# Performance work log

Hardware: AMD Instinct MI355X
Metric: run time of the kernel (lower is better)

The kernel has to match this reference:

```python
import jax, jax.numpy as jnp
import numpy as np

B, K = 4, 128
V_IN, V_OUT = 256, 256
E_IN, E_OUT = 512, 512
P_PE, T_PE = 200, 100
HEADS = 16  # c_atten_head


def _lin(key, din, dout):
    kw, kb = jax.random.split(key)
    W = jax.random.normal(kw, (din, dout), jnp.float32) / np.sqrt(din).astype(np.float32)
    b = jax.random.normal(kb, (dout,), jnp.float32) * 0.01
    return W, b


def setup_inputs() -> dict:
    key = jax.random.key(0)
    ks = jax.random.split(key, 14)
    v_f = jax.random.normal(ks[0], (B, K, V_IN), jnp.float32)
    e_f = jax.random.normal(ks[1], (B, K * K, E_IN), jnp.float32)
    p_pe = jax.random.normal(ks[2], (B, K, P_PE), jnp.float32)
    t_pe = jax.random.normal(ks[3], (B, T_PE), jnp.float32)
    e_agg_mask = (jax.random.uniform(ks[4], (B, K, K)) > 0.1).astype(jnp.float32)
    v_agg_mask = (jax.random.uniform(ks[5], (B, K)) > 0.1).astype(jnp.float32)
    W_vpe, b_vpe = _lin(ks[6], V_IN + P_PE + T_PE, V_IN)
    W_epe, b_epe = _lin(ks[7], E_IN + T_PE, E_IN)
    W_ev1, b_ev1 = _lin(ks[8], E_IN + 2 * V_IN, E_OUT)
    W_ev2, b_ev2 = _lin(ks[9], E_OUT, E_OUT)
    W_q, b_q = _lin(ks[10], V_IN, E_OUT)
    W_k, b_k = _lin(ks[11], V_IN, E_OUT)
    W_self, b_self = _lin(ks[12], V_IN, E_OUT)
    W_out, b_out = _lin(ks[13], 2 * E_OUT, V_OUT)
    return dict(v_f=v_f, e_f=e_f, p_pe=p_pe, t_pe=t_pe,
                e_agg_mask=e_agg_mask, v_agg_mask=v_agg_mask,
                W_vpe=W_vpe, b_vpe=b_vpe, W_epe=W_epe, b_epe=b_epe,
                W_ev1=W_ev1, b_ev1=b_ev1, W_ev2=W_ev2, b_ev2=b_ev2,
                W_q=W_q, b_q=b_q, W_k=W_k, b_k=b_k,
                W_self=W_self, b_self=b_self, W_out=W_out, b_out=b_out)


def reference(v_f, e_f, p_pe, t_pe, e_agg_mask, v_agg_mask,
              W_vpe, b_vpe, W_epe, b_epe, W_ev1, b_ev1, W_ev2, b_ev2,
              W_q, b_q, W_k, b_k, W_self, b_self, W_out, b_out):
    silu = jax.nn.silu
    # PE binding
    t_v = jnp.broadcast_to(t_pe[:, None, :], (B, K, T_PE))
    v = silu(jnp.concatenate([v_f, p_pe, t_v], -1) @ W_vpe + b_vpe)          # (B,K,V_IN)
    t_e = jnp.broadcast_to(t_pe[:, None, :], (B, K * K, T_PE))
    e = silu(jnp.concatenate([e_f, t_e], -1) @ W_epe + b_epe)                # (B,K*K,E_IN)
    # dense all-pairs node features -> edge values
    pair = jnp.concatenate([jnp.broadcast_to(v[:, :, None, :], (B, K, K, V_IN)),
                            jnp.broadcast_to(v[:, None, :, :], (B, K, K, V_IN))], -1)
    ev_in = jnp.concatenate([pair.reshape(B, K * K, 2 * V_IN), e], -1)
    e_value = silu(ev_in @ W_ev1 + b_ev1) @ W_ev2 + b_ev2                     # (B,K*K,E_OUT)
    agg_e = e_value.reshape(B, K, K, E_OUT)
    # elementwise-multiply / head-sum attention
    q = v @ W_q + b_q                                                         # (B,K,E_OUT)
    k = v @ W_k + b_k
    att = (q[:, :, None, :] * k[:, None, :, :]).reshape(B, K, K, E_OUT // HEADS, HEADS)
    att = att.sum(-1, keepdims=True) / np.float32(np.sqrt(HEADS * 3.0))       # (B,K,K,G,1)
    a = jax.nn.sigmoid(att) * e_agg_mask[..., None, None]
    a = a / (a.sum(2, keepdims=True) + 1e-6)
    a = jnp.broadcast_to(a, (B, K, K, E_OUT // HEADS, HEADS)).reshape(B, K, K, E_OUT)
    agg_v = (a * agg_e).sum(2)                                                # (B,K,E_OUT)
    v2 = agg_v + silu(v @ W_self + b_self)
    # masked max-pool over nodes
    pooled = (v2 - 1e9 * (1.0 - v_agg_mask)[..., None]).max(1, keepdims=True)
    pooled = jnp.broadcast_to(pooled, (B, K, E_OUT))
    v_out = silu(jnp.concatenate([v2, pooled], -1) @ W_out + b_out)           # (B,K,V_OUT)
    return v_out, e_value
```

## Files before the change

kernel.cpp:

```cpp
#include <hip/hip_runtime.h>

typedef unsigned short ushort_t;
typedef __attribute__((ext_vector_type(8))) short bf16x8;
typedef __attribute__((ext_vector_type(4))) float f32x4;

__device__ __forceinline__ ushort_t f2bf(float f) {
    union { float f; unsigned u; } v; v.f = f;
    unsigned r = v.u + 0x7FFFu + ((v.u >> 16) & 1u);
    return (ushort_t)(r >> 16);
}
__device__ __forceinline__ float siluf(float x) { return x / (1.f + __expf(-x)); }
__device__ __forceinline__ float sigm(float x)  { return 1.f / (1.f + __expf(-x)); }

__device__ __forceinline__ void gl2lds16(const void* g, void* l) {
    __builtin_amdgcn_global_load_lds(
        (__attribute__((address_space(1))) void*)(const_cast<void*>(g)),
        (__attribute__((address_space(3))) void*)(l), 16, 0, 0);
}


__global__ void k_prep(const float* t_pe, const float* W_vpe, const float* b_vpe,
                       const float* W_epe, const float* b_epe,
                       float* c_v, float* c_e) {
    int b = blockIdx.x, t = threadIdx.x;
    {
        float acc = b_epe[t];
        for (int u = 0; u < 100; ++u) acc += t_pe[b*100+u] * W_epe[(512+u)*512 + t];
        c_e[b*512 + t] = acc;
    }
    if (t < 256) {
        float acc = b_vpe[t];
        for (int u = 0; u < 100; ++u) acc += t_pe[b*100+u] * W_vpe[(456+u)*256 + t];
        c_v[b*256 + t] = acc;
    }
}

__global__ void k_transpose(const float* W_epe, const float* W_ev1, const float* W_ev2,
                            ushort_t* WT_epe, ushort_t* WT_c, ushort_t* WT_ev2) {
    int n = blockIdx.x;
    int mat = blockIdx.y;
    const float* src; ushort_t* dst;
    if (mat == 0)      { src = W_epe;            dst = WT_epe; }
    else if (mat == 1) { src = W_ev1 + 512*512;  dst = WT_c;   }
    else               { src = W_ev2;            dst = WT_ev2; }
    for (int k = threadIdx.x; k < 512; k += 256)
        dst[n*512 + k] = f2bf(src[k*512 + n]);
}

__global__ __launch_bounds__(256) void k_cvt(const float* src, ushort_t* dst) {
    size_t id = (size_t)blockIdx.x * 256 + threadIdx.x;
    const float4* s = (const float4*)src + id * 2;
    float4 a = s[0], b = s[1];
    ushort4* d = (ushort4*)dst + id * 2;
    d[0] = make_ushort4(f2bf(a.x), f2bf(a.y), f2bf(a.z), f2bf(a.w));
    d[1] = make_ushort4(f2bf(b.x), f2bf(b.y), f2bf(b.z), f2bf(b.w));
}

__global__ void k_node_v(const float* v_f, const float* p_pe, const float* W_vpe,
                         const float* c_v, float* v) {
    __shared__ float rv[4][256];
    __shared__ float rp[4][200];
    int r0 = blockIdx.x * 4, t = threadIdx.x;
    for (int rr = 0; rr < 4; ++rr) {
        rv[rr][t] = v_f[(r0+rr)*256 + t];
        if (t < 200) rp[rr][t] = p_pe[(r0+rr)*200 + t];
    }
    __syncthreads();
    int b = r0 >> 7;
    float acc[4];
    float cv = c_v[b*256 + t];
    for (int rr = 0; rr < 4; ++rr) acc[rr] = cv;
    for (int k = 0; k < 256; ++k) {
        float w = W_vpe[k*256 + t];
        #pragma unroll
        for (int rr = 0; rr < 4; ++rr) acc[rr] += rv[rr][k] * w;
    }
    for (int k = 0; k < 200; ++k) {
        float w = W_vpe[(256+k)*256 + t];
        #pragma unroll
        for (int rr = 0; rr < 4; ++rr) acc[rr] += rp[rr][k] * w;
    }
    for (int rr = 0; rr < 4; ++rr) v[(r0+rr)*256 + t] = siluf(acc[rr]);
}

__global__ void k_node_proj(const float* v,
                            const float* W_q, const float* b_q,
                            const float* W_k, const float* b_k,
                            const float* W_self, const float* b_self,
                            const float* W_ev1, const float* b_ev1,
                            float* q, float* kk, float* vs, float* P, float* Q) {
    __shared__ float rv[4][256];
    int r0 = blockIdx.x * 4, which = blockIdx.y, t = threadIdx.x;
    for (int rr = 0; rr < 4; ++rr) rv[rr][t] = v[(r0+rr)*256 + t];
    __syncthreads();
    const float* W; const float* bias = nullptr; float* out; bool do_silu = false;
    if (which == 0)      { W = W_q;    bias = b_q;    out = q;  }
    else if (which == 1) { W = W_k;    bias = b_k;    out = kk; }
    else if (which == 2) { W = W_self; bias = b_self; out = vs; do_silu = true; }
    else if (which == 3) { W = W_ev1;  bias = b_ev1;  out = P;  }
    else                 { W = W_ev1 + 256*512;       out = Q;  }
    float acc[4][2] = {};
    for (int k = 0; k < 256; ++k) {
        float w0 = W[k*512 + t];
        float w1 = W[k*512 + t + 256];
        #pragma unroll
        for (int rr = 0; rr < 4; ++rr) {
            acc[rr][0] += rv[rr][k] * w0;
            acc[rr][1] += rv[rr][k] * w1;
        }
    }
    float bb0 = bias ? bias[t] : 0.f;
    float bb1 = bias ? bias[t + 256] : 0.f;
    for (int rr = 0; rr < 4; ++rr) {
        float x0 = acc[rr][0] + bb0;
        float x1 = acc[rr][1] + bb1;
        if (do_silu) { x0 = siluf(x0); x1 = siluf(x1); }
        out[(r0+rr)*512 + t]       = x0;
        out[(r0+rr)*512 + t + 256] = x1;
    }
}

__global__ __launch_bounds__(256) void k_attw(const float* q, const float* kmat,
                                              const float* emask, float* anorm) {
    int bi = blockIdx.x; int b = bi >> 7, i = bi & 127;
    int t = threadIdx.x;
    __shared__ __align__(16) float qrow[512];
    __shared__ float s[128][33];
    __shared__ float invd[32];
    qrow[t]       = q[(size_t)bi*512 + t];
    qrow[t + 256] = q[(size_t)bi*512 + t + 256];
    __syncthreads();
    {
        int j = t >> 1, g0 = (t & 1) * 16;
        const float* kr = kmat + ((size_t)b*128 + j) * 512;
        float msk = emask[(size_t)b*16384 + i*128 + j];
        for (int gg = 0; gg < 16; ++gg) {
            int g = g0 + gg;
            const float4* k4 = (const float4*)(kr + g*16);
            const float4* q4 = (const float4*)(qrow + g*16);
            float acc = 0.f;
            #pragma unroll
            for (int c = 0; c < 4; ++c) {
                float4 kv = k4[c], qv = q4[c];
                acc += kv.x*qv.x + kv.y*qv.y + kv.z*qv.z + kv.w*qv.w;
            }
            s[j][g] = sigm(acc * 0.14433756729740645f) * msk;
        }
    }
    __syncthreads();
    if (t < 32) {
        float d = 1e-6f;
        for (int j = 0; j < 128; ++j) d += s[j][t];
        invd[t] = 1.f / d;
    }
    __syncthreads();
    float* dst = anorm + (size_t)bi * 4096;
    for (int idx = t; idx < 4096; idx += 256) {
        int j = idx >> 5, g = idx & 31;
        dst[idx] = s[j][g] * invd[g];
    }
}

template <int MODE>
__global__ __launch_bounds__(256) void k_gemm(const ushort_t* A, const ushort_t* BT,
                                              const float* e0, const float* e1,
                                              const float* e2,
                                              ushort_t* out16, float* out32,
                                              float* v2out) {
    __shared__ __align__(16) ushort_t As[128*32];
    __shared__ __align__(16) ushort_t Bs[128*32];
    __shared__ float aw[(MODE == 2) ? 4096 : 4];
    __shared__ float red[(MODE == 2) ? 256 : 4];

    int lin = blockIdx.x;
    int xcd = lin & 7, idx = lin >> 3;
    int mt = xcd * 64 + (idx >> 2);
    int nt = idx & 3;
    int m0 = mt * 128, n0 = nt * 128;
    int t = threadIdx.x;
    int wv = t >> 6, lane = t & 63;
    int wm = (wv >> 1) * 64, wn = (wv & 1) * 64;
    int ml = lane & 15, quad = lane >> 4;
    f32x4 acc[4][4] = {};

    if (MODE == 2) {
        const float4* src = (const float4*)(e1 + (size_t)mt * 4096);
        float4* dst = (float4*)aw;
        for (int i = t; i < 1024; i += 256) dst[i] = src[i];
    }

    int srow = t >> 2, sseg = t & 3;
    const ushort_t* gA0 = A + (size_t)(m0 + srow) * 512 + sseg * 8;
    const ushort_t* gA1 = A + (size_t)(m0 + 64 + srow) * 512 + sseg * 8;
    const ushort_t* gB0 = BT + (size_t)(n0 + srow) * 512 + sseg * 8;
    const ushort_t* gB1 = BT + (size_t)(n0 + 64 + srow) * 512 + sseg * 8;
    ushort_t* lA0 = As + wv * 512;
    ushort_t* lA1 = As + 2048 + wv * 512;
    ushort_t* lB0 = Bs + wv * 512;
    ushort_t* lB1 = Bs + 2048 + wv * 512;

    for (int kk = 0; kk < 512; kk += 32) {
        gl2lds16(gA0 + kk, lA0);
        gl2lds16(gA1 + kk, lA1);
        gl2lds16(gB0 + kk, lB0);
        gl2lds16(gB1 + kk, lB1);
        __syncthreads();
        bf16x8 a[4], b[4];
        #pragma unroll
        for (int tm = 0; tm < 4; ++tm)
            a[tm] = *(const bf16x8*)(As + (wm + tm*16 + ml) * 32 + quad * 8);
        #pragma unroll
        for (int tn = 0; tn < 4; ++tn)
            b[tn] = *(const bf16x8*)(Bs + (wn + tn*16 + ml) * 32 + quad * 8);
        #pragma unroll
        for (int tm = 0; tm < 4; ++tm)
            #pragma unroll
            for (int tn = 0; tn < 4; ++tn)
                acc[tm][tn] = __builtin_amdgcn_mfma_f32_16x16x32_bf16(a[tm], b[tn], acc[tm][tn], 0, 0, 0);
        __syncthreads();
    }

    if (MODE == 2) {
        float partial[4] = {0.f, 0.f, 0.f, 0.f};
        #pragma unroll
        for (int tm = 0; tm < 4; ++tm)
            #pragma unroll
            for (int tn = 0; tn < 4; ++tn)
                #pragma unroll
                for (int r = 0; r < 4; ++r) {
                    int j  = wm + tm*16 + quad*4 + r;
                    int gn = n0 + wn + tn*16 + ml;
                    float x = acc[tm][tn][r] + e0[gn];
                    out32[((size_t)m0 + j) * 512 + gn] = x;
                    partial[tn] += aw[j * 32 + (gn >> 4)] * x;
                }
        #pragma unroll
        for (int tn = 0; tn < 4; ++tn) {
            float p = partial[tn];
            p += __shfl_down(p, 32);
            p += __shfl_down(p, 16);
            if (quad == 0 && lane < 16) red[wv * 64 + tn * 16 + ml] = p;
        }
        __syncthreads();
        if (t < 128) {
            int c = t, half = c >> 6, cl = c & 63;
            float tot = red[half * 64 + cl] + red[(half + 2) * 64 + cl];
            size_t o = (size_t)mt * 512 + n0 + c;
            v2out[o] = tot + e2[o];
        }
    } else {
        #pragma unroll
        for (int tm = 0; tm < 4; ++tm)
            #pragma unroll
            for (int tn = 0; tn < 4; ++tn)
                #pragma unroll
                for (int r = 0; r < 4; ++r) {
                    int gm = m0 + wm + tm*16 + quad*4 + r;
                    int gn = n0 + wn + tn*16 + ml;
                    float x = acc[tm][tn][r];
                    if (MODE == 0) {
                        x += e0[(gm >> 14) * 512 + gn];
                    } else {
                        int b_ = gm >> 14, ij = gm & 16383, i = ij >> 7, j = ij & 127;
                        x += e0[(size_t)((b_ << 7) + i) * 512 + gn]
                           + e1[(size_t)((b_ << 7) + j) * 512 + gn];
                    }
                    out16[(size_t)gm * 512 + gn] = f2bf(siluf(x));
                }
    }
}

__global__ void k_pool(const float* v2, const float* vmask, const float* W_out,
                       const float* b_out, float* cpool) {
    int b = blockIdx.x, t = threadIdx.x;
    __shared__ float pooled[512];
    for (int d = t; d < 512; d += 256) {
        float m = -1e30f;
        for (int i = 0; i < 128; ++i) {
            float val = v2[((size_t)(b*128 + i))*512 + d] - 1e9f * (1.f - vmask[b*128 + i]);
            m = fmaxf(m, val);
        }
        pooled[d] = m;
    }
    __syncthreads();
    float acc = b_out[t];
    for (int d = 0; d < 512; ++d) acc += pooled[d] * W_out[(512 + d)*256 + t];
    cpool[b*256 + t] = acc;
}

__global__ void k_node_out(const float* v2, const float* W_out, const float* cpool,
                           float* out) {
    __shared__ float rv[4][512];
    int r0 = blockIdx.x * 4, t = threadIdx.x;
    for (int rr = 0; rr < 4; ++rr) {
        rv[rr][t]       = v2[(size_t)(r0+rr)*512 + t];
        rv[rr][t + 256] = v2[(size_t)(r0+rr)*512 + t + 256];
    }
    __syncthreads();
    int b = r0 >> 7;
    float acc[4];
    float cp = cpool[b*256 + t];
    for (int rr = 0; rr < 4; ++rr) acc[rr] = cp;
    for (int k = 0; k < 512; ++k) {
        float w = W_out[k*256 + t];
        #pragma unroll
        for (int rr = 0; rr < 4; ++rr) acc[rr] += rv[rr][k] * w;
    }
    for (int rr = 0; rr < 4; ++rr) out[(r0+rr)*256 + t] = siluf(acc[rr]);
}

extern "C" void kernel_launch(void* const* d_in, const int* in_sizes, int n_in,
                              void* d_out, int out_size, void* d_ws, size_t ws_size,
                              hipStream_t stream) {
    const float* v_f    = (const float*)d_in[0];
    const float* e_f    = (const float*)d_in[1];
    const float* p_pe   = (const float*)d_in[2];
    const float* t_pe   = (const float*)d_in[3];
    const float* emask  = (const float*)d_in[4];
    const float* vmask  = (const float*)d_in[5];
    const float* W_vpe  = (const float*)d_in[6];
    const float* b_vpe  = (const float*)d_in[7];
    const float* W_epe  = (const float*)d_in[8];
    const float* b_epe  = (const float*)d_in[9];
    const float* W_ev1  = (const float*)d_in[10];
    const float* b_ev1  = (const float*)d_in[11];
    const float* W_ev2  = (const float*)d_in[12];
    const float* b_ev2  = (const float*)d_in[13];
    const float* W_q    = (const float*)d_in[14];
    const float* b_q    = (const float*)d_in[15];
    const float* W_k    = (const float*)d_in[16];
    const float* b_k    = (const float*)d_in[17];
    const float* W_self = (const float*)d_in[18];
    const float* b_self = (const float*)d_in[19];
    const float* W_out  = (const float*)d_in[20];
    const float* b_out  = (const float*)d_in[21];

    float* out_v = (float*)d_out;
    float* out_e = (float*)d_out + 131072;

    char* w = (char*)d_ws;
    ushort_t* WT_epe = (ushort_t*)w; w += 512*512*2;
    ushort_t* WT_c   = (ushort_t*)w; w += 512*512*2;
    ushort_t* WT_ev2 = (ushort_t*)w; w += 512*512*2;
    float* c_v   = (float*)w; w += 4*256*4;
    float* c_e   = (float*)w; w += 4*512*4;
    float* v     = (float*)w; w += 512*256*4;
    float* qbuf  = (float*)w; w += 512*512*4;
    float* kbuf  = (float*)w; w += 512*512*4;
    float* vsbuf = (float*)w; w += 512*512*4;
    float* Pbuf  = (float*)w; w += 512*512*4;
    float* Qbuf  = (float*)w; w += 512*512*4;
    float* v2buf = (float*)w; w += 512*512*4;
    float* cpool = (float*)w; w += 4*256*4;
    float* anorm = (float*)w; w += (size_t)4*128*128*32*4;
    ushort_t* e16  = (ushort_t*)w; w += (size_t)65536*512*2;
    ushort_t* ef16 = (ushort_t*)w; w += (size_t)65536*512*2;
    ushort_t* h16  = ef16;

    k_prep<<<4, 512, 0, stream>>>(t_pe, W_vpe, b_vpe, W_epe, b_epe, c_v, c_e);
    k_transpose<<<dim3(512, 3), 256, 0, stream>>>(W_epe, W_ev1, W_ev2, WT_epe, WT_c, WT_ev2);
    k_node_v<<<128, 256, 0, stream>>>(v_f, p_pe, W_vpe, c_v, v);
    k_node_proj<<<dim3(128, 5), 256, 0, stream>>>(v, W_q, b_q, W_k, b_k, W_self, b_self,
                                                  W_ev1, b_ev1, qbuf, kbuf, vsbuf, Pbuf, Qbuf);
    k_attw<<<512, 256, 0, stream>>>(qbuf, kbuf, emask, anorm);
    k_cvt<<<16384, 256, 0, stream>>>(e_f, ef16);
    k_gemm<0><<<2048, 256, 0, stream>>>(ef16, WT_epe, c_e, nullptr, nullptr, e16, nullptr, nullptr);
    k_gemm<1><<<2048, 256, 0, stream>>>(e16, WT_c, Pbuf, Qbuf, nullptr, h16, nullptr, nullptr);
    k_gemm<2><<<2048, 256, 0, stream>>>(h16, WT_ev2, b_ev2, anorm, vsbuf, nullptr, out_e, v2buf);
    k_pool<<<4, 256, 0, stream>>>(v2buf, vmask, W_out, b_out, cpool);
    k_node_out<<<128, 256, 0, stream>>>(v2buf, W_out, cpool, out_v);
}
```

Before: 671.3 us.

## Fuse fp32 conversion into GEMM, double-buffer K loop, merge small kernels

The first GEMM now reads fp32 edge features directly and converts them to bf16 while staging into shared memory, which removes the separate conversion pass and its bf16 round trip through global memory. The GEMM K loop is restructured into 64-wide steps with double-buffered shared memory, so loads for the next step overlap the MFMAs of the current one and half as many barriers are needed. Epilogue bias and row loads are hoisted out of the inner loops. The prep and transpose kernels are merged, and the pool and output kernels are merged, with every output block recomputing the pooled max and its projection redundantly. Shared memory per block grows to 64KB, which may reduce occupancy.

```diff
diff --git a/kernel.cpp b/kernel.cpp
--- a/kernel.cpp
+++ b/kernel.cpp
@@ -18,42 +18,34 @@
         (__attribute__((address_space(3))) void*)(l), 16, 0, 0);
 }
 
-
-__global__ void k_prep(const float* t_pe, const float* W_vpe, const float* b_vpe,
-                       const float* W_epe, const float* b_epe,
-                       float* c_v, float* c_e) {
-    int b = blockIdx.x, t = threadIdx.x;
-    {
-        float acc = b_epe[t];
-        for (int u = 0; u < 100; ++u) acc += t_pe[b*100+u] * W_epe[(512+u)*512 + t];
-        c_e[b*512 + t] = acc;
-    }
-    if (t < 256) {
-        float acc = b_vpe[t];
-        for (int u = 0; u < 100; ++u) acc += t_pe[b*100+u] * W_vpe[(456+u)*256 + t];
-        c_v[b*256 + t] = acc;
-    }
-}
-
-__global__ void k_transpose(const float* W_epe, const float* W_ev1, const float* W_ev2,
-                            ushort_t* WT_epe, ushort_t* WT_c, ushort_t* WT_ev2) {
-    int n = blockIdx.x;
-    int mat = blockIdx.y;
+__global__ void k_pt(const float* W_epe, const float* W_ev1, const float* W_ev2,
+                     const float* t_pe, const float* W_vpe, const float* b_vpe,
+                     const float* b_epe,
+                     ushort_t* WT_epe, ushort_t* WT_c, ushort_t* WT_ev2,
+                     float* c_v, float* c_e) {
+    int n = blockIdx.x, mat = blockIdx.y, t = threadIdx.x;
+    if (mat == 3) {
+        if (n < 4) {
+            int b = n;
+            for (int col = t; col < 512; col += 256) {
+                float acc = b_epe[col];
+                for (int u = 0; u < 100; ++u) acc += t_pe[b*100+u] * W_epe[(512+u)*512 + col];
+                c_e[b*512 + col] = acc;
+            }
+            {
+                float acc = b_vpe[t];
+                for (int u = 0; u < 100; ++u) acc += t_pe[b*100+u] * W_vpe[(456+u)*256 + t];
+                c_v[b*256 + t] = acc;
+            }
+        }
+        return;
+    }
     const float* src; ushort_t* dst;
     if (mat == 0)      { src = W_epe;            dst = WT_epe; }
     else if (mat == 1) { src = W_ev1 + 512*512;  dst = WT_c;   }
     else               { src = W_ev2;            dst = WT_ev2; }
-    for (int k = threadIdx.x; k < 512; k += 256)
+    for (int k = t; k < 512; k += 256)
         dst[n*512 + k] = f2bf(src[k*512 + n]);
-}
-
-__global__ __launch_bounds__(256) void k_cvt(const float* src, ushort_t* dst) {
-    size_t id = (size_t)blockIdx.x * 256 + threadIdx.x;
-    const float4* s = (const float4*)src + id * 2;
-    float4 a = s[0], b = s[1];
-    ushort4* d = (ushort4*)dst + id * 2;
-    d[0] = make_ushort4(f2bf(a.x), f2bf(a.y), f2bf(a.z), f2bf(a.w));
-    d[1] = make_ushort4(f2bf(b.x), f2bf(b.y), f2bf(b.z), f2bf(b.w));
 }
 
 __global__ void k_node_v(const float* v_f, const float* p_pe, const float* W_vpe,
@@ -162,16 +154,12 @@
 }
 
 template <int MODE>
-__global__ __launch_bounds__(256) void k_gemm(const ushort_t* A, const ushort_t* BT,
+__global__ __launch_bounds__(256) void k_gemm(const void* Aptr, const ushort_t* BT,
                                               const float* e0, const float* e1,
                                               const float* e2,
                                               ushort_t* out16, float* out32,
                                               float* v2out) {
-    __shared__ __align__(16) ushort_t As[128*32];
-    __shared__ __align__(16) ushort_t Bs[128*32];
-    __shared__ float aw[(MODE == 2) ? 4096 : 4];
-    __shared__ float red[(MODE == 2) ? 256 : 4];
-
+    __shared__ __align__(16) ushort_t smem[32768];
     int lin = blockIdx.x;
     int xcd = lin & 7, idx = lin >> 3;
     int mt = xcd * 64 + (idx >> 2);
@@ -183,44 +171,96 @@
     int ml = lane & 15, quad = lane >> 4;
     f32x4 acc[4][4] = {};
 
+    int brow = t >> 2, bseg = t & 3;
+    const ushort_t* gB = BT + (size_t)(n0 + brow) * 512 + bseg * 8;
+    const ushort_t* gA16 = (const ushort_t*)Aptr + (size_t)(m0 + brow) * 512 + bseg * 8;
+    const float*    gA32 = (const float*)Aptr + (size_t)(m0 + (t >> 4)) * 512 + (t & 15) * 4;
+
+    float4 f[8];
+    int ahalf = (t >> 3) & 1;
+    int acol  = (t & 7) * 4;
+
+    auto issueB = [&](int it, int d) {
+        int kk = it * 64;
+        #pragma unroll
+        for (int s = 0; s < 2; ++s)
+            #pragma unroll
+            for (int g = 0; g < 2; ++g)
+                gl2lds16(gB + (size_t)g * 64 * 512 + kk + s * 32,
+                         smem + 16384 + d * 8192 + s * 4096 + g * 2048 + wv * 512);
+    };
+    auto issueA16 = [&](int it, int d) {
+        int kk = it * 64;
+        #pragma unroll
+        for (int s = 0; s < 2; ++s)
+            #pragma unroll
+            for (int g = 0; g < 2; ++g)
+                gl2lds16(gA16 + (size_t)g * 64 * 512 + kk + s * 32,
+                         smem + d * 8192 + s * 4096 + g * 2048 + wv * 512);
+    };
+    auto loadA32 = [&](int it) {
+        int kk = it * 64;
+        #pragma unroll
+        for (int j = 0; j < 8; ++j)
+            f[j] = *(const float4*)(gA32 + (size_t)(j * 16) * 512 + kk);
+    };
+    auto writeA32 = [&](int d) {
+        #pragma unroll
+        for (int j = 0; j < 8; ++j) {
+            int row = (t >> 4) + j * 16;
+            ushort_t* dst = smem + d * 8192 + ahalf * 4096 + row * 32 + acol;
+            float4 v4 = f[j];
+            *(ushort4*)dst = make_ushort4(f2bf(v4.x), f2bf(v4.y), f2bf(v4.z), f2bf(v4.w));
+        }
+    };
+    auto compute = [&](int d) {
+        #pragma unroll
+        for (int s = 0; s < 2; ++s) {
+            bf16x8 a[4], b[4];
+            #pragma unroll
+            for (int tm = 0; tm < 4; ++tm)
+                a[tm] = *(const bf16x8*)(smem + d * 8192 + s * 4096 + (wm + tm*16 + ml) * 32 + quad * 8);
+            #pragma unroll
+            for (int tn = 0; tn < 4; ++tn)
+                b[tn] = *(const bf16x8*)(smem + 16384 + d * 8192 + s * 4096 + (wn + tn*16 + ml) * 32 + quad * 8);
+            #pragma unroll
+            for (int tm = 0; tm < 4; ++tm)
+                #pragma unroll
+                for (int tn = 0; tn < 4; ++tn)
+                    acc[tm][tn] = __builtin_amdgcn_mfma_f32_16x16x32_bf16(a[tm], b[tn], acc[tm][tn], 0, 0, 0);
+        }
+    };
+
+    if (MODE == 0) { issueB(0, 0); loadA32(0); writeA32(0); }
+    else           { issueB(0, 0); issueA16(0, 0); }
+
+    for (int it = 0; it < 8; ++it) {
+        __syncthreads();
+        int nd = (it + 1) & 1;
+        if (MODE == 0) {
+            if (it < 7) { issueB(it + 1, nd); loadA32(it + 1); }
+            compute(it & 1);
+            if (it < 7) writeA32(nd);
+        } else {
+            if (it < 7) { issueB(it + 1, nd); issueA16(it + 1, nd); }
+            compute(it & 1);
+        }
+    }
+
+    int gn0 = n0 + wn + ml;
     if (MODE == 2) {
-        const float4* src = (const float4*)(e1 + (size_t)mt * 4096);
-        float4* dst = (float4*)aw;
-        for (int i = t; i < 1024; i += 256) dst[i] = src[i];
-    }
-
-    int srow = t >> 2, sseg = t & 3;
-    const ushort_t* gA0 = A + (size_t)(m0 + srow) * 512 + sseg * 8;
-    const ushort_t* gA1 = A + (size_t)(m0 + 64 + srow) * 512 + sseg * 8;
-    const ushort_t* gB0 = BT + (size_t)(n0 + srow) * 512 + sseg * 8;
-    const ushort_t* gB1 = BT + (size_t)(n0 + 64 + srow) * 512 + sseg * 8;
-    ushort_t* lA0 = As + wv * 512;
-    ushort_t* lA1 = As + 2048 + wv * 512;
-    ushort_t* lB0 = Bs + wv * 512;
-    ushort_t* lB1 = Bs + 2048 + wv * 512;
-
-    for (int kk = 0; kk < 512; kk += 32) {
-        gl2lds16(gA0 + kk, lA0);
-        gl2lds16(gA1 + kk, lA1);
-        gl2lds16(gB0 + kk, lB0);
-        gl2lds16(gB1 + kk, lB1);
         __syncthreads();
-        bf16x8 a[4], b[4];
-        #pragma unroll
-        for (int tm = 0; tm < 4; ++tm)
-            a[tm] = *(const bf16x8*)(As + (wm + tm*16 + ml) * 32 + quad * 8);
-        #pragma unroll
-        for (int tn = 0; tn < 4; ++tn)
-            b[tn] = *(const bf16x8*)(Bs + (wn + tn*16 + ml) * 32 + quad * 8);
-        #pragma unroll
-        for (int tm = 0; tm < 4; ++tm)
-            #pragma unroll
-            for (int tn = 0; tn < 4; ++tn)
-                acc[tm][tn] = __builtin_amdgcn_mfma_f32_16x16x32_bf16(a[tm], b[tn], acc[tm][tn], 0, 0, 0);
+        float* aw  = (float*)smem;
+        float* red = aw + 4096;
+        {
+            const float4* src = (const float4*)(e1 + (size_t)mt * 4096);
+            float4* dw = (float4*)aw;
+            for (int i2 = t; i2 < 1024; i2 += 256) dw[i2] = src[i2];
+        }
         __syncthreads();
-    }
-
-    if (MODE == 2) {
+        float bv[4];
+        #pragma unroll
+        for (int tn = 0; tn < 4; ++tn) bv[tn] = e0[gn0 + tn*16];
         float partial[4] = {0.f, 0.f, 0.f, 0.f};
         #pragma unroll
         for (int tm = 0; tm < 4; ++tm)
@@ -229,8 +269,8 @@
                 #pragma unroll
                 for (int r = 0; r < 4; ++r) {
                     int j  = wm + tm*16 + quad*4 + r;
-                    int gn = n0 + wn + tn*16 + ml;
-                    float x = acc[tm][tn][r] + e0[gn];
+                    int gn = gn0 + tn*16;
+                    float x = acc[tm][tn][r] + bv[tn];
                     out32[((size_t)m0 + j) * 512 + gn] = x;
                     partial[tn] += aw[j * 32 + (gn >> 4)] * x;
                 }
@@ -248,58 +288,66 @@
             size_t o = (size_t)mt * 512 + n0 + c;
             v2out[o] = tot + e2[o];
         }
-    } else {
+    } else if (MODE == 1) {
+        int bi = mt;
+        int brow0 = (bi >> 7) << 7;
+        float Pv[4];
+        #pragma unroll
+        for (int tn = 0; tn < 4; ++tn) Pv[tn] = e0[(size_t)bi * 512 + gn0 + tn*16];
         #pragma unroll
         for (int tm = 0; tm < 4; ++tm)
             #pragma unroll
             for (int tn = 0; tn < 4; ++tn)
                 #pragma unroll
                 for (int r = 0; r < 4; ++r) {
-                    int gm = m0 + wm + tm*16 + quad*4 + r;
-                    int gn = n0 + wn + tn*16 + ml;
-                    float x = acc[tm][tn][r];
-                    if (MODE == 0) {
-                        x += e0[(gm >> 14) * 512 + gn];
-                    } else {
-                        int b_ = gm >> 14, ij = gm & 16383, i = ij >> 7, j = ij & 127;
-                        x += e0[(size_t)((b_ << 7) + i) * 512 + gn]
-                           + e1[(size_t)((b_ << 7) + j) * 512 + gn];
-                    }
-                    out16[(size_t)gm * 512 + gn] = f2bf(siluf(x));
+                    int j  = wm + tm*16 + quad*4 + r;
+                    int gn = gn0 + tn*16;
+                    float x = acc[tm][tn][r] + Pv[tn]
+                            + e1[(size_t)(brow0 + j) * 512 + gn];
+                    out16[((size_t)m0 + j) * 512 + gn] = f2bf(siluf(x));
                 }
-    }
-}
-
-__global__ void k_pool(const float* v2, const float* vmask, const float* W_out,
-                       const float* b_out, float* cpool) {
-    int b = blockIdx.x, t = threadIdx.x;
+    } else {
+        int b_ = mt >> 7;
+        float cv[4];
+        #pragma unroll
+        for (int tn = 0; tn < 4; ++tn) cv[tn] = e0[b_ * 512 + gn0 + tn*16];
+        #pragma unroll
+        for (int tm = 0; tm < 4; ++tm)
+            #pragma unroll
+            for (int tn = 0; tn < 4; ++tn)
+                #pragma unroll
+                for (int r = 0; r < 4; ++r) {
+                    int j  = wm + tm*16 + quad*4 + r;
+                    int gn = gn0 + tn*16;
+                    float x = acc[tm][tn][r] + cv[tn];
+                    out16[((size_t)m0 + j) * 512 + gn] = f2bf(siluf(x));
+                }
+    }
+}
+
+__global__ __launch_bounds__(256) void k_out(const float* v2, const float* vmask,
+                                             const float* W_out, const float* b_out,
+                                             float* out) {
     __shared__ float pooled[512];
-    for (int d = t; d < 512; d += 256) {
-        float m = -1e30f;
-        for (int i = 0; i < 128; ++i) {
-            float val = v2[((size_t)(b*128 + i))*512 + d] - 1e9f * (1.f - vmask[b*128 + i]);
-            m = fmaxf(m, val);
-        }
-        pooled[d] = m;
-    }
-    __syncthreads();
-    float acc = b_out[t];
-    for (int d = 0; d < 512; ++d) acc += pooled[d] * W_out[(512 + d)*256 + t];
-    cpool[b*256 + t] = acc;
-}
-
-__global__ void k_node_out(const float* v2, const float* W_out, const float* cpool,
-                           float* out) {
     __shared__ float rv[4][512];
-    int r0 = blockIdx.x * 4, t = threadIdx.x;
+    __shared__ float vm[128];
+    int r0 = blockIdx.x * 4, t = threadIdx.x, b = r0 >> 7;
+    if (t < 128) vm[t] = -1e9f * (1.f - vmask[b*128 + t]);
     for (int rr = 0; rr < 4; ++rr) {
         rv[rr][t]       = v2[(size_t)(r0+rr)*512 + t];
         rv[rr][t + 256] = v2[(size_t)(r0+rr)*512 + t + 256];
     }
     __syncthreads();
-    int b = r0 >> 7;
+    for (int d = t; d < 512; d += 256) {
+        float m = -1e30f;
+        for (int i = 0; i < 128; ++i)
+            m = fmaxf(m, v2[((size_t)(b*128 + i))*512 + d] + vm[i]);
+        pooled[d] = m;
+    }
+    __syncthreads();
+    float cp = b_out[t];
+    for (int d = 0; d < 512; ++d) cp += pooled[d] * W_out[(512 + d)*256 + t];
     float acc[4];
-    float cp = cpool[b*256 + t];
     for (int rr = 0; rr < 4; ++rr) acc[rr] = cp;
     for (int k = 0; k < 512; ++k) {
         float w = W_out[k*256 + t];
@@ -351,22 +399,18 @@
     float* Pbuf  = (float*)w; w += 512*512*4;
     float* Qbuf  = (float*)w; w += 512*512*4;
     float* v2buf = (float*)w; w += 512*512*4;
-    float* cpool = (float*)w; w += 4*256*4;
     float* anorm = (float*)w; w += (size_t)4*128*128*32*4;
-    ushort_t* e16  = (ushort_t*)w; w += (size_t)65536*512*2;
-    ushort_t* ef16 = (ushort_t*)w; w += (size_t)65536*512*2;
-    ushort_t* h16  = ef16;
-
-    k_prep<<<4, 512, 0, stream>>>(t_pe, W_vpe, b_vpe, W_epe, b_epe, c_v, c_e);
-    k_transpose<<<dim3(512, 3), 256, 0, stream>>>(W_epe, W_ev1, W_ev2, WT_epe, WT_c, WT_ev2);
+    ushort_t* e16 = (ushort_t*)w; w += (size_t)65536*512*2;
+    ushort_t* h16 = (ushort_t*)w; w += (size_t)65536*512*2;
+
+    k_pt<<<dim3(512, 4), 256, 0, stream>>>(W_epe, W_ev1, W_ev2, t_pe, W_vpe, b_vpe, b_epe,
+                                           WT_epe, WT_c, WT_ev2, c_v, c_e);
     k_node_v<<<128, 256, 0, stream>>>(v_f, p_pe, W_vpe, c_v, v);
     k_node_proj<<<dim3(128, 5), 256, 0, stream>>>(v, W_q, b_q, W_k, b_k, W_self, b_self,
                                                   W_ev1, b_ev1, qbuf, kbuf, vsbuf, Pbuf, Qbuf);
     k_attw<<<512, 256, 0, stream>>>(qbuf, kbuf, emask, anorm);
-    k_cvt<<<16384, 256, 0, stream>>>(e_f, ef16);
-    k_gemm<0><<<2048, 256, 0, stream>>>(ef16, WT_epe, c_e, nullptr, nullptr, e16, nullptr, nullptr);
+    k_gemm<0><<<2048, 256, 0, stream>>>(e_f, WT_epe, c_e, nullptr, nullptr, e16, nullptr, nullptr);
     k_gemm<1><<<2048, 256, 0, stream>>>(e16, WT_c, Pbuf, Qbuf, nullptr, h16, nullptr, nullptr);
     k_gemm<2><<<2048, 256, 0, stream>>>(h16, WT_ev2, b_ev2, anorm, vsbuf, nullptr, out_e, v2buf);
-    k_pool<<<4, 256, 0, stream>>>(v2buf, vmask, W_out, b_out, cpool);
-    k_node_out<<<128, 256, 0, stream>>>(v2buf, W_out, cpool, out_v);
-}
+    k_out<<<128, 256, 0, stream>>>(v2buf, vmask, W_out, b_out, out_v);
+}
```

After: 648.3 us. 1.04x faster.
